# Kernel tuning notes

Hardware: AMD Instinct MI355X
Metric: run time of the kernel (lower is better)

## Reference

```python
import jax, jax.numpy as jnp
import numpy as np

B, Q, K = 4, 256, 1024          # batch, query_len, key_len
DQ, DK, DV, H = 512, 512, 512, 256  # query/key/value dims, num_hiddens


def setup_inputs() -> dict:
    key = jax.random.key(0)
    ks = jax.random.split(key, 7)
    return {
        "queries": jax.random.normal(ks[0], (B, Q, DQ), jnp.float32),
        "keys": jax.random.normal(ks[1], (B, K, DK), jnp.float32),
        "values": jax.random.normal(ks[2], (B, K, DV), jnp.float32),
        "valid_lens": jax.random.randint(ks[3], (B,), 1, K + 1),
        "Wq": jax.random.normal(ks[4], (H, DQ), jnp.float32) / np.sqrt(DQ).astype(np.float32),
        "Wk": jax.random.normal(ks[5], (H, DK), jnp.float32) / np.sqrt(DK).astype(np.float32),
        "wv": jax.random.normal(ks[6], (H,), jnp.float32) / np.sqrt(H).astype(np.float32),
    }


def reference(queries, keys, values, valid_lens, Wq, Wk, wv):
    # Linear projections (bias=False), torch Linear weight layout (out, in)
    q = jnp.einsum("bqd,hd->bqh", queries, Wq)          # (B, Q, H)
    k = jnp.einsum("bkd,hd->bkh", keys, Wk)             # (B, K, H)
    # Broadcast add -> tanh -> scalar score per (q, k) pair
    feats = jnp.tanh(q[:, :, None, :] + k[:, None, :, :])  # (B, Q, K, H)
    scores = jnp.einsum("bqkh,h->bqk", feats, wv)           # (B, Q, K)
    # masked_softmax with 1D valid_lens: mask applies along key axis per batch
    kv_len = scores.shape[-1]
    mask = jnp.arange(kv_len)[None, None, :] < valid_lens[:, None, None]  # (B,1,K)
    scores = jnp.where(mask, scores, jnp.float32(-1e6))
    attn = jax.nn.softmax(scores, axis=-1)               # (B, Q, K)
    # dropout is identity in eval mode
    return jnp.einsum("bqk,bkv->bqv", attn, values)      # (B, Q, DV)
```

## Files before the change

### kernel.cpp

```cpp
#include <hip/hip_runtime.h>
#include <stdint.h>


#define NB 4
#define NQ 256
#define NK 1024
#define ND 512
#define NH 256
#define QROWS 4
#define PJR 16
#define PJH 64

#define C2L2E 2.8853900817779268f
#define L2E   1.4426950408889634f

typedef float v2f __attribute__((ext_vector_type(2)));

__device__ void ff_vldec(const int* p, int* v) {
  bool ok = true;
  for (int i = 0; i < 4; ++i) { int x = p[i]; if (x < 1 || x > NK) ok = false; }
  if (ok) { for (int i = 0; i < 4; ++i) v[i] = p[i]; return; }
  ok = true;
  for (int i = 0; i < 4; ++i) {
    if (p[2 * i + 1] != 0) ok = false;
    int x = p[2 * i]; if (x < 1 || x > NK) ok = false;
  }
  if (ok) { for (int i = 0; i < 4; ++i) v[i] = p[2 * i]; return; }
  ok = true;
  for (int i = 0; i < 4; ++i) {
    union { int i; float f; } u; u.i = p[i];
    if (!(u.f >= 1.0f && u.f <= 1024.0f && u.f == floorf(u.f))) ok = false;
  }
  if (ok) {
    for (int i = 0; i < 4; ++i) { union { int i; float f; } u; u.i = p[i]; v[i] = (int)u.f; }
    return;
  }
  ok = true;
  for (int i = 0; i < 4; ++i) {
    union { long long l; double d; } u;
    u.l = ((long long)p[2 * i + 1] << 32) | (unsigned int)p[2 * i];
    if (!(u.d >= 1.0 && u.d <= 1024.0 && u.d == floor(u.d))) ok = false;
  }
  if (ok) {
    for (int i = 0; i < 4; ++i) {
      union { long long l; double d; } u;
      u.l = ((long long)p[2 * i + 1] << 32) | (unsigned int)p[2 * i];
      v[i] = (int)u.d;
    }
    return;
  }
  const uint16_t* hh = (const uint16_t*)p;
  const short*    s  = (const short*)p;
  ok = true;
  for (int i = 0; i < 4; ++i) { int x = s[i]; if (x < 1 || x > NK) ok = false; }
  if (ok) { for (int i = 0; i < 4; ++i) v[i] = s[i]; return; }
  ok = true;
  for (int i = 0; i < 4; ++i) {
    union { uint16_t u; _Float16 h; } u; u.u = hh[i];
    float f = (float)u.h;
    if (!(f >= 1.0f && f <= 1024.0f && f == floorf(f))) ok = false;
  }
  if (ok) {
    for (int i = 0; i < 4; ++i) {
      union { uint16_t u; _Float16 h; } u; u.u = hh[i];
      v[i] = (int)(float)u.h;
    }
    return;
  }
  ok = true;
  for (int i = 0; i < 4; ++i) {
    union { uint32_t u; float f; } u; u.u = ((uint32_t)hh[i]) << 16;
    if (!(u.f >= 1.0f && u.f <= 1028.0f)) ok = false;
  }
  if (ok) {
    for (int i = 0; i < 4; ++i) {
      union { uint32_t u; float f; } u; u.u = ((uint32_t)hh[i]) << 16;
      int x = (int)(u.f + 0.5f); if (x > NK) x = NK; v[i] = x;
    }
    return;
  }
  for (int i = 0; i < 4; ++i) v[i] = NK;
}

__global__ __launch_bounds__(256) void ff_wt(
    const float* __restrict__ Wq, const float* __restrict__ Wk,
    float* __restrict__ WTq, float* __restrict__ WTk)
{
  const int idx = blockIdx.x * 256 + threadIdx.x;
  const int d4 = idx & 127, h = idx >> 7;
  const float* src = blockIdx.y ? Wk : Wq;
  float*       dst = blockIdx.y ? WTk : WTq;
  float4 w = *(const float4*)(src + (size_t)h * ND + d4 * 4);
  w.x *= C2L2E; w.y *= C2L2E; w.z *= C2L2E; w.w *= C2L2E;
  *(float4*)(dst + ((size_t)d4 * NH + h) * 4) = w;
}

__global__ __launch_bounds__(256) void ff_proj(
    const float* __restrict__ q_in, const float* __restrict__ k_in,
    const float* __restrict__ WTq, const float* __restrict__ WTk,
    float* __restrict__ qp, float* __restrict__ kp)
{
  __shared__ float xs[PJR * ND];
  const int t  = threadIdx.x;
  const int rg = blockIdx.x >> 2;
  const int h0 = (blockIdx.x & 3) * PJH;
  const int gr0 = rg * PJR;
  const bool isq = gr0 < NB * NQ;
  const float* xin = isq ? (q_in + (size_t)gr0 * ND)
                         : (k_in + (size_t)(gr0 - NB * NQ) * ND);
  const float4* wt4 = (const float4*)(isq ? WTq : WTk);

  #pragma unroll
  for (int i = 0; i < 8; ++i)
    ((float4*)xs)[t + 256 * i] = ((const float4*)xin)[t + 256 * i];
  __syncthreads();

  const int L  = t & 63;
  const int rw = t >> 6;
  float a0 = 0.f, a1 = 0.f, a2 = 0.f, a3 = 0.f;
  const float4* xr = (const float4*)xs + (size_t)(4 * rw) * 128;

  #pragma unroll 4
  for (int d4 = 0; d4 < ND / 4; ++d4) {
    float4 w  = wt4[(size_t)d4 * NH + h0 + L];
    float4 x0 = xr[d4];
    float4 x1 = xr[128 + d4];
    float4 x2 = xr[256 + d4];
    float4 x3 = xr[384 + d4];
    a0 += w.x*x0.x + w.y*x0.y + w.z*x0.z + w.w*x0.w;
    a1 += w.x*x1.x + w.y*x1.y + w.z*x1.z + w.w*x1.w;
    a2 += w.x*x2.x + w.y*x2.y + w.z*x2.z + w.w*x2.w;
    a3 += w.x*x3.x + w.y*x3.y + w.z*x3.z + w.w*x3.w;
  }
  a0 = __builtin_amdgcn_exp2f(a0);
  a1 = __builtin_amdgcn_exp2f(a1);
  a2 = __builtin_amdgcn_exp2f(a2);
  a3 = __builtin_amdgcn_exp2f(a3);

  if (isq) {
    const int h = h0 + L;
    float* o = qp + (size_t)(gr0 + 4 * rw) * NH + h;
    o[0] = a0; o[NH] = a1; o[2 * NH] = a2; o[3 * NH] = a3;
  } else {
    __syncthreads();
    float* trs = xs;
    *(float4*)&trs[L * 16 + 4 * rw] = make_float4(a0, a1, a2, a3);
    __syncthreads();
    const int kl = t & 15, jl = t >> 4;
    const int g0 = gr0 - NB * NQ;
    const int bb = g0 >> 10, kg0 = g0 & (NK - 1);
    const int j0 = (blockIdx.x & 3) * 16;
    float4 o4 = make_float4(trs[(4*jl+0)*16 + kl], trs[(4*jl+1)*16 + kl],
                            trs[(4*jl+2)*16 + kl], trs[(4*jl+3)*16 + kl]);
    ((float4*)kp)[((size_t)bb * 64 + j0 + jl) * 1024 + kg0 + kl] = o4;
  }
}

__global__ __launch_bounds__(1024, 8) void ff_attn_s(
    const float* __restrict__ qp, const float* __restrict__ kp,
    const int* __restrict__ vlraw, const float* __restrict__ wvp,
    float* __restrict__ Eg, float* __restrict__ Sg)
{
  __shared__ float  qs[QROWS * NH];
  __shared__ float4 wspp[NH / 2];
  __shared__ float  el[512 * 4];
  __shared__ float  psum[32];

  const int t  = threadIdx.x;
  const int kh = blockIdx.x;
  const int q4 = blockIdx.y;
  const int b  = blockIdx.z;

  qs[t] = qp[((size_t)b * NQ + q4 * QROWS) * NH + t];
  if (t < NH / 2) {
    float w0 = wvp[2 * t], w1 = wvp[2 * t + 1];
    wspp[t] = make_float4(-2.0f * w0, -2.0f * w1, -2.0f * (w0 + w1), 0.0f);
  }
  __syncthreads();

  int vls[4];
  ff_vldec(vlraw, vls);
  const int vl = vls[b];

  const int l  = t & 63, w = t >> 6;
  const int hs = l >> 4, kl = l & 15;
  const int kw = w & 7,  rh = w >> 3;
  const int kk = kw * 16 + kl;
  const int k0 = kh * 512 + kk * 4;

  v2f acc0 = {0.f,0.f}, acc1 = {0.f,0.f}, acc2 = {0.f,0.f}, acc3 = {0.f,0.f};
  {
    const float4* kvp = (const float4*)kp + (size_t)b * 64 * 1024 + k0;
    const float* q0p = qs + (2 * rh) * NH;
    const float* q1p = qs + (2 * rh + 1) * NH;

    for (int jj = 0; jj < 16; ++jj) {
      const int j = hs * 16 + jj;
      const float4* kj = kvp + ((size_t)j << 10);
      float4 K0 = kj[0], K1 = kj[1], K2 = kj[2], K3 = kj[3];
      float4 A0 = *(const float4*)(q0p + 4 * j);
      float4 A1 = *(const float4*)(q1p + 4 * j);
      float4 wa = wspp[2 * j];
      float4 wb = wspp[2 * j + 1];
      v2f one; one.x = 1.0f; one.y = 1.0f;

#define FF_PAIRK(K4, ACC)                                                  \
      {                                                                    \
        v2f a, b2, D, N, w0v, w1v, rD;                                     \
        a.x  = A0.x * K4.x; a.y  = A1.x * K4.x;                            \
        b2.x = A0.y * K4.y; b2.y = A1.y * K4.y;                            \
        D = (one + a) * (one + b2);                                        \
        N.x = wa.z; N.y = wa.z;                                            \
        w0v.x = wa.x; w0v.y = wa.x;                                        \
        w1v.x = wa.y; w1v.y = wa.y;                                        \
        N += w0v * b2; N += w1v * a;                                       \
        rD.x = __builtin_amdgcn_rcpf(D.x);                                 \
        rD.y = __builtin_amdgcn_rcpf(D.y);                                 \
        ACC += N * rD;                                                     \
        a.x  = A0.z * K4.z; a.y  = A1.z * K4.z;                            \
        b2.x = A0.w * K4.w; b2.y = A1.w * K4.w;                            \
        D = (one + a) * (one + b2);                                        \
        N.x = wb.z; N.y = wb.z;                                            \
        w0v.x = wb.x; w0v.y = wb.x;                                        \
        w1v.x = wb.y; w1v.y = wb.y;                                        \
        N += w0v * b2; N += w1v * a;                                       \
        rD.x = __builtin_amdgcn_rcpf(D.x);                                 \
        rD.y = __builtin_amdgcn_rcpf(D.y);                                 \
        ACC += N * rD;                                                     \
      }
      FF_PAIRK(K0, acc0)
      FF_PAIRK(K1, acc1)
      FF_PAIRK(K2, acc2)
      FF_PAIRK(K3, acc3)
#undef FF_PAIRK
    }
  }

#define FF_RED(v)                                                          \
  v.x += __shfl_xor(v.x, 16); v.x += __shfl_xor(v.x, 32);                  \
  v.y += __shfl_xor(v.y, 16); v.y += __shfl_xor(v.y, 32);
  FF_RED(acc0) FF_RED(acc1) FF_RED(acc2) FF_RED(acc3)
#undef FF_RED

  float ex0, ey0, ex1, ey1, ex2, ey2, ex3, ey3;
  {
    const bool m0 = (k0 + 0) < vl, m1 = (k0 + 1) < vl;
    const bool m2 = (k0 + 2) < vl, m3 = (k0 + 3) < vl;
    ex0 = m0 ? __builtin_amdgcn_exp2f(acc0.x * L2E) : 0.f;
    ey0 = m0 ? __builtin_amdgcn_exp2f(acc0.y * L2E) : 0.f;
    ex1 = m1 ? __builtin_amdgcn_exp2f(acc1.x * L2E) : 0.f;
    ey1 = m1 ? __builtin_amdgcn_exp2f(acc1.y * L2E) : 0.f;
    ex2 = m2 ? __builtin_amdgcn_exp2f(acc2.x * L2E) : 0.f;
    ey2 = m2 ? __builtin_amdgcn_exp2f(acc2.y * L2E) : 0.f;
    ex3 = m3 ? __builtin_amdgcn_exp2f(acc3.x * L2E) : 0.f;
    ey3 = m3 ? __builtin_amdgcn_exp2f(acc3.y * L2E) : 0.f;
  }

  if (hs == 0) {
    const int klc = kk * 4;
    el[(klc + 0) * 4 + 2 * rh] = ex0; el[(klc + 0) * 4 + 2 * rh + 1] = ey0;
    el[(klc + 1) * 4 + 2 * rh] = ex1; el[(klc + 1) * 4 + 2 * rh + 1] = ey1;
    el[(klc + 2) * 4 + 2 * rh] = ex2; el[(klc + 2) * 4 + 2 * rh + 1] = ey2;
    el[(klc + 3) * 4 + 2 * rh] = ex3; el[(klc + 3) * 4 + 2 * rh + 1] = ey3;
  }
  {
    float sl = (hs == 0) ? ((ex0 + ex1) + (ex2 + ex3)) : 0.f;
    float sh = (hs == 0) ? ((ey0 + ey1) + (ey2 + ey3)) : 0.f;
    for (int o = 32; o; o >>= 1) { sl += __shfl_xor(sl, o); sh += __shfl_xor(sh, o); }
    if (l == 0) { psum[w * 2] = sl; psum[w * 2 + 1] = sh; }
  }
  __syncthreads();

  if (t < 512)
    ((float4*)Eg)[((size_t)b * 64 + q4) * NK + kh * 512 + t]
        = *(const float4*)&el[t * 4];

  if (t < 4) {
    const int c = t & 1, base = (t >> 1) * 8;
    float S = 0.f;
    #pragma unroll
    for (int kw2 = 0; kw2 < 8; ++kw2) S += psum[(base + kw2) * 2 + c];
    Sg[(((size_t)b * 64 + q4) * 4 + t) * 2 + kh] = S;
  }
}

__global__ __launch_bounds__(256) void ff_pv(
    const float* __restrict__ vals, const float* __restrict__ Eg,
    const float* __restrict__ Sg, const int* __restrict__ vlraw,
    float* __restrict__ out)
{
  __shared__ float part[8 * 4 * 64];
  const int t  = threadIdx.x;
  const int ct = blockIdx.x;
  const int q4 = blockIdx.y;
  const int b  = blockIdx.z;

  int vls[4];
  ff_vldec(vlraw, vls);
  const int vl = vls[b];

  const int cl = t & 31, kq = t >> 5;
  const int c  = ct * 64 + cl * 2;
  const int k0 = kq * 128;
  int klen = vl - k0; klen = klen < 0 ? 0 : (klen > 128 ? 128 : klen);

  const float*  vb = vals + (size_t)b * NK * ND + (size_t)k0 * ND + c;
  const float4* ep = (const float4*)Eg + ((size_t)b * 64 + q4) * NK + k0;

  v2f a0 = {0.f,0.f}, a1 = {0.f,0.f}, a2 = {0.f,0.f}, a3 = {0.f,0.f};
  #pragma unroll 4
  for (int k = 0; k < klen; ++k) {
    float4 E = ep[k];
    v2f v = *(const v2f*)(vb + (size_t)k * ND);
    v2f e;
    e.x = E.x; e.y = E.x; a0 += e * v;
    e.x = E.y; e.y = E.y; a1 += e * v;
    e.x = E.z; e.y = E.z; a2 += e * v;
    e.x = E.w; e.y = E.w; a3 += e * v;
  }
  {
    float* pp = &part[(size_t)(kq * 4) * 64 + cl * 2];
    *(v2f*)(pp      ) = a0;
    *(v2f*)(pp + 64 ) = a1;
    *(v2f*)(pp + 128) = a2;
    *(v2f*)(pp + 192) = a3;
  }
  __syncthreads();
  {
    const int r = t >> 6, cc = t & 63;
    float s = 0.f;
    #pragma unroll
    for (int q = 0; q < 8; ++q) s += part[(size_t)(q * 4 + r) * 64 + cc];
    const size_t sb = ((size_t)b * 64 + q4) * 4 + r;
    const float S = Sg[sb * 2] + Sg[sb * 2 + 1];
    out[((size_t)b * NQ + q4 * QROWS + r) * ND + ct * 64 + cc] = s / S;
  }
}

__global__ __launch_bounds__(1024) void ff_attn(
    const float* __restrict__ qp, const float* __restrict__ kp,
    const float* __restrict__ vals, const int* __restrict__ vlraw,
    const float* __restrict__ wvp, float* __restrict__ out)
{
  __shared__ float qs[QROWS * NH];
  __shared__ float ws[NH];
  __shared__ float st[NK * QROWS];
  __shared__ float pm[16], psm[16];
  __shared__ float part[4 * QROWS * ND];

  const int t  = threadIdx.x;
  const int q0 = blockIdx.x * QROWS;
  const int b  = blockIdx.y;

  {
    const float* qsrc = qp + ((size_t)b * NQ + q0) * NH;
    qs[t] = qsrc[t];
    if (t < NH) ws[t] = -2.0f * wvp[t];
  }
  __syncthreads();

  int vls[4];
  ff_vldec(vlraw, vls);
  const int vl = vls[b];

  float sc[4] = {0.f, 0.f, 0.f, 0.f};
  {
    const float4* kvp = (const float4*)kp + ((size_t)b * 64) * 1024 + t;
    for (int j = 0; j < 64; ++j) {
      float4 K4 = kvp[(size_t)j << 10];
      const float* wj = &ws[4 * j];
      #pragma unroll
      for (int r = 0; r < 4; ++r) {
        const float* qr = &qs[r * NH + 4 * j];
        sc[r] += wj[0] * __builtin_amdgcn_rcpf(1.0f + qr[0] * K4.x);
        sc[r] += wj[1] * __builtin_amdgcn_rcpf(1.0f + qr[1] * K4.y);
        sc[r] += wj[2] * __builtin_amdgcn_rcpf(1.0f + qr[2] * K4.z);
        sc[r] += wj[3] * __builtin_amdgcn_rcpf(1.0f + qr[3] * K4.w);
      }
    }
  }
  {
    const bool okm = (t < vl);
    *(float4*)&st[t * 4] = make_float4(okm ? sc[0] : -1e6f, okm ? sc[1] : -1e6f,
                                       okm ? sc[2] : -1e6f, okm ? sc[3] : -1e6f);
  }
  __syncthreads();

  {
    const int wid = t >> 6, lane = t & 63;
    const int row = wid >> 2, seg = wid & 3;
    const int kb = seg * 256 + lane;
    float v0 = st[(kb      ) * 4 + row];
    float v1 = st[(kb +  64) * 4 + row];
    float v2 = st[(kb + 128) * 4 + row];
    float v3 = st[(kb + 192) * 4 + row];
    float m = fmaxf(fmaxf(v0, v1), fmaxf(v2, v3));
    for (int o = 32; o; o >>= 1) m = fmaxf(m, __shfl_xor(m, o));
    if (lane == 0) pm[wid] = m;
    __syncthreads();
    m = fmaxf(fmaxf(pm[row*4+0], pm[row*4+1]), fmaxf(pm[row*4+2], pm[row*4+3]));
    float e0 = __builtin_amdgcn_exp2f((v0 - m) * L2E);
    float e1 = __builtin_amdgcn_exp2f((v1 - m) * L2E);
    float e2 = __builtin_amdgcn_exp2f((v2 - m) * L2E);
    float e3 = __builtin_amdgcn_exp2f((v3 - m) * L2E);
    float sm = e0 + e1 + e2 + e3;
    for (int o = 32; o; o >>= 1) sm += __shfl_xor(sm, o);
    if (lane == 0) psm[wid] = sm;
    __syncthreads();
    const float S = psm[row*4+0] + psm[row*4+1] + psm[row*4+2] + psm[row*4+3];
    const float rr = 1.0f / S;
    st[(kb      ) * 4 + row] = e0 * rr;
    st[(kb +  64) * 4 + row] = e1 * rr;
    st[(kb + 128) * 4 + row] = e2 * rr;
    st[(kb + 192) * 4 + row] = e3 * rr;
  }
  __syncthreads();

  {
    const int kq = t >> 8, c2 = (t & 255) * 2;
    const float* vb = vals + (size_t)b * NK * ND + c2;
    v2f o0 = {0.f,0.f}, o1 = {0.f,0.f}, o2 = {0.f,0.f}, o3 = {0.f,0.f};
    const int k0 = kq * 256;
    #pragma unroll 8
    for (int k = k0; k < k0 + 256; ++k) {
      v2f vv = *(const v2f*)(vb + (size_t)k * ND);
      float4 a = *(const float4*)&st[k * 4];
      v2f ax; ax.x = a.x; ax.y = a.x;
      v2f ay; ay.x = a.y; ay.y = a.y;
      v2f az; az.x = a.z; az.y = a.z;
      v2f aw; aw.x = a.w; aw.y = a.w;
      o0 += ax * vv; o1 += ay * vv; o2 += az * vv; o3 += aw * vv;
    }
    float* pp = &part[(size_t)kq * QROWS * ND + c2];
    *(v2f*)(pp         ) = o0;
    *(v2f*)(pp +     ND) = o1;
    *(v2f*)(pp + 2 * ND) = o2;
    *(v2f*)(pp + 3 * ND) = o3;
  }
  __syncthreads();
  {
    const int r = t >> 8, c2 = (t & 255) * 2;
    const float* pp = &part[(size_t)r * ND + c2];
    v2f s = {0.f, 0.f};
    #pragma unroll
    for (int kq = 0; kq < 4; ++kq) s += *(const v2f*)(pp + (size_t)kq * QROWS * ND);
    *(v2f*)(out + ((size_t)b * NQ + q0 + r) * ND + c2) = s;
  }
}

extern "C" void kernel_launch(void* const* d_in, const int* in_sizes, int n_in,
                              void* d_out, int out_size, void* d_ws, size_t ws_size,
                              hipStream_t stream) {
  const float* queries = (const float*)d_in[0];
  const float* keys    = (const float*)d_in[1];
  const float* values  = (const float*)d_in[2];
  const int*   vlens   = (const int*)d_in[3];
  const float* Wq      = (const float*)d_in[4];
  const float* Wk      = (const float*)d_in[5];
  const float* wv      = (const float*)d_in[6];
  float* out = (float*)d_out;

  float* qp  = (float*)d_ws;
  float* kp  = qp  + (size_t)NB * NQ * NH;
  float* wtq = kp  + (size_t)NB * NH * NK;
  float* wtk = wtq + (size_t)(ND / 4) * NH * 4;
  float* Eg  = wtk + (size_t)(ND / 4) * NH * 4;
  float* Sg  = Eg  + (size_t)NB * 64 * NK * 4;
  const size_t need = ((size_t)(Sg - (float*)d_ws) + NB * 64 * 4 * 2) * sizeof(float);

  ff_wt  <<<dim3(128, 2), 256, 0, stream>>>(Wq, Wk, wtq, wtk);
  ff_proj<<<dim3((NB * (NQ + NK) / PJR) * (NH / PJH)), 256, 0, stream>>>(
      queries, keys, wtq, wtk, qp, kp);
  if (ws_size >= need) {
    ff_attn_s<<<dim3(2, NQ / QROWS, NB), 1024, 0, stream>>>(
        qp, kp, vlens, wv, Eg, Sg);
    ff_pv<<<dim3(8, NQ / QROWS, NB), 256, 0, stream>>>(
        values, Eg, Sg, vlens, out);
  } else {
    ff_attn<<<dim3(NQ / QROWS, NB), 1024, 0, stream>>>(
        qp, kp, values, vlens, wv, out);
  }
}
```

Before: 174.7 us.

## Widen per-block tiles in projection and PV kernels, pad LDS to avoid conflicts

The projection kernel now computes 128 hidden columns per block instead of 64, so each staged input row tile is reused across twice as many outputs and half as many blocks reload it. The PV kernel handles two query groups per block, reusing each loaded value vector for eight query rows and halving value-matrix traffic. The LDS transpose buffers in the projection and score kernels are padded (stride 17 and 5) to reduce bank conflicts. In exchange, register pressure rises and there are fewer blocks to fill the GPU.

Result: slower. 183.8 us (+5.2%).

```diff
diff --git a/kernel.cpp b/kernel.cpp
--- a/kernel.cpp
+++ b/kernel.cpp
@@ -9,7 +9,6 @@
 #define NH 256
 #define QROWS 4
 #define PJR 16
-#define PJH 64
 
 #define C2L2E 2.8853900817779268f
 #define L2E   1.4426950408889634f
@@ -102,8 +101,8 @@
 {
   __shared__ float xs[PJR * ND];
   const int t  = threadIdx.x;
-  const int rg = blockIdx.x >> 2;
-  const int h0 = (blockIdx.x & 3) * PJH;
+  const int rg = blockIdx.x >> 1;
+  const int hh = blockIdx.x & 1;
   const int gr0 = rg * PJR;
   const bool isq = gr0 < NB * NQ;
   const float* xin = isq ? (q_in + (size_t)gr0 * ND)
@@ -117,42 +116,58 @@
 
   const int L  = t & 63;
   const int rw = t >> 6;
-  float a0 = 0.f, a1 = 0.f, a2 = 0.f, a3 = 0.f;
+  float ac0[4], ac1[4];
+  #pragma unroll
+  for (int r = 0; r < 4; ++r) { ac0[r] = 0.f; ac1[r] = 0.f; }
   const float4* xr = (const float4*)xs + (size_t)(4 * rw) * 128;
+  const int hbase = hh * 128 + L;
 
   #pragma unroll 4
   for (int d4 = 0; d4 < ND / 4; ++d4) {
-    float4 w  = wt4[(size_t)d4 * NH + h0 + L];
+    float4 w0 = wt4[(size_t)d4 * NH + hbase];
+    float4 w1 = wt4[(size_t)d4 * NH + hbase + 64];
     float4 x0 = xr[d4];
     float4 x1 = xr[128 + d4];
     float4 x2 = xr[256 + d4];
     float4 x3 = xr[384 + d4];
-    a0 += w.x*x0.x + w.y*x0.y + w.z*x0.z + w.w*x0.w;
-    a1 += w.x*x1.x + w.y*x1.y + w.z*x1.z + w.w*x1.w;
-    a2 += w.x*x2.x + w.y*x2.y + w.z*x2.z + w.w*x2.w;
-    a3 += w.x*x3.x + w.y*x3.y + w.z*x3.z + w.w*x3.w;
-  }
-  a0 = __builtin_amdgcn_exp2f(a0);
-  a1 = __builtin_amdgcn_exp2f(a1);
-  a2 = __builtin_amdgcn_exp2f(a2);
-  a3 = __builtin_amdgcn_exp2f(a3);
+    ac0[0] += w0.x*x0.x + w0.y*x0.y + w0.z*x0.z + w0.w*x0.w;
+    ac0[1] += w0.x*x1.x + w0.y*x1.y + w0.z*x1.z + w0.w*x1.w;
+    ac0[2] += w0.x*x2.x + w0.y*x2.y + w0.z*x2.z + w0.w*x2.w;
+    ac0[3] += w0.x*x3.x + w0.y*x3.y + w0.z*x3.z + w0.w*x3.w;
+    ac1[0] += w1.x*x0.x + w1.y*x0.y + w1.z*x0.z + w1.w*x0.w;
+    ac1[1] += w1.x*x1.x + w1.y*x1.y + w1.z*x1.z + w1.w*x1.w;
+    ac1[2] += w1.x*x2.x + w1.y*x2.y + w1.z*x2.z + w1.w*x2.w;
+    ac1[3] += w1.x*x3.x + w1.y*x3.y + w1.z*x3.z + w1.w*x3.w;
+  }
+  #pragma unroll
+  for (int r = 0; r < 4; ++r) {
+    ac0[r] = __builtin_amdgcn_exp2f(ac0[r]);
+    ac1[r] = __builtin_amdgcn_exp2f(ac1[r]);
+  }
 
   if (isq) {
-    const int h = h0 + L;
-    float* o = qp + (size_t)(gr0 + 4 * rw) * NH + h;
-    o[0] = a0; o[NH] = a1; o[2 * NH] = a2; o[3 * NH] = a3;
+    float* o = qp + (size_t)(gr0 + 4 * rw) * NH + hh * 128 + L;
+    #pragma unroll
+    for (int r = 0; r < 4; ++r) {
+      o[(size_t)r * NH]      = ac0[r];
+      o[(size_t)r * NH + 64] = ac1[r];
+    }
   } else {
     __syncthreads();
     float* trs = xs;
-    *(float4*)&trs[L * 16 + 4 * rw] = make_float4(a0, a1, a2, a3);
+    *(float4*)&trs[(L     ) * 17 + 4 * rw] = make_float4(ac0[0], ac0[1], ac0[2], ac0[3]);
+    *(float4*)&trs[(L + 64) * 17 + 4 * rw] = make_float4(ac1[0], ac1[1], ac1[2], ac1[3]);
     __syncthreads();
-    const int kl = t & 15, jl = t >> 4;
+    const int kl = t & 15, jl2 = t >> 4;
     const int g0 = gr0 - NB * NQ;
     const int bb = g0 >> 10, kg0 = g0 & (NK - 1);
-    const int j0 = (blockIdx.x & 3) * 16;
-    float4 o4 = make_float4(trs[(4*jl+0)*16 + kl], trs[(4*jl+1)*16 + kl],
-                            trs[(4*jl+2)*16 + kl], trs[(4*jl+3)*16 + kl]);
-    ((float4*)kp)[((size_t)bb * 64 + j0 + jl) * 1024 + kg0 + kl] = o4;
+    #pragma unroll
+    for (int it = 0; it < 2; ++it) {
+      const int jl = jl2 + 16 * it;
+      float4 o4 = make_float4(trs[(4*jl+0)*17 + kl], trs[(4*jl+1)*17 + kl],
+                              trs[(4*jl+2)*17 + kl], trs[(4*jl+3)*17 + kl]);
+      ((float4*)kp)[((size_t)bb * 64 + hh * 32 + jl) * 1024 + kg0 + kl] = o4;
+    }
   }
 }
 
@@ -163,7 +178,7 @@
 {
   __shared__ float  qs[QROWS * NH];
   __shared__ float4 wspp[NH / 2];
-  __shared__ float  el[512 * 4];
+  __shared__ float  el[512 * 5];
   __shared__ float  psum[32];
 
   const int t  = threadIdx.x;
@@ -258,10 +273,10 @@
 
   if (hs == 0) {
     const int klc = kk * 4;
-    el[(klc + 0) * 4 + 2 * rh] = ex0; el[(klc + 0) * 4 + 2 * rh + 1] = ey0;
-    el[(klc + 1) * 4 + 2 * rh] = ex1; el[(klc + 1) * 4 + 2 * rh + 1] = ey1;
-    el[(klc + 2) * 4 + 2 * rh] = ex2; el[(klc + 2) * 4 + 2 * rh + 1] = ey2;
-    el[(klc + 3) * 4 + 2 * rh] = ex3; el[(klc + 3) * 4 + 2 * rh + 1] = ey3;
+    el[(klc + 0) * 5 + 2 * rh] = ex0; el[(klc + 0) * 5 + 2 * rh + 1] = ey0;
+    el[(klc + 1) * 5 + 2 * rh] = ex1; el[(klc + 1) * 5 + 2 * rh + 1] = ey1;
+    el[(klc + 2) * 5 + 2 * rh] = ex2; el[(klc + 2) * 5 + 2 * rh + 1] = ey2;
+    el[(klc + 3) * 5 + 2 * rh] = ex3; el[(klc + 3) * 5 + 2 * rh + 1] = ey3;
   }
   {
     float sl = (hs == 0) ? ((ex0 + ex1) + (ex2 + ex3)) : 0.f;
@@ -271,9 +286,11 @@
   }
   __syncthreads();
 
-  if (t < 512)
+  if (t < 512) {
+    const float* e = &el[t * 5];
     ((float4*)Eg)[((size_t)b * 64 + q4) * NK + kh * 512 + t]
-        = *(const float4*)&el[t * 4];
+        = make_float4(e[0], e[1], e[2], e[3]);
+  }
 
   if (t < 4) {
     const int c = t & 1, base = (t >> 1) * 8;
@@ -289,10 +306,10 @@
     const float* __restrict__ Sg, const int* __restrict__ vlraw,
     float* __restrict__ out)
 {
-  __shared__ float part[8 * 4 * 64];
+  __shared__ float part[8 * 8 * 64];
   const int t  = threadIdx.x;
   const int ct = blockIdx.x;
-  const int q4 = blockIdx.y;
+  const int qg = blockIdx.y;
   const int b  = blockIdx.z;
 
   int vls[4];
@@ -304,36 +321,52 @@
   const int k0 = kq * 128;
   int klen = vl - k0; klen = klen < 0 ? 0 : (klen > 128 ? 128 : klen);
 
-  const float*  vb = vals + (size_t)b * NK * ND + (size_t)k0 * ND + c;
-  const float4* ep = (const float4*)Eg + ((size_t)b * 64 + q4) * NK + k0;
+  const float*  vb  = vals + (size_t)b * NK * ND + (size_t)k0 * ND + c;
+  const float4* epa = (const float4*)Eg + ((size_t)b * 64 + qg * 2    ) * NK + k0;
+  const float4* epb = (const float4*)Eg + ((size_t)b * 64 + qg * 2 + 1) * NK + k0;
 
   v2f a0 = {0.f,0.f}, a1 = {0.f,0.f}, a2 = {0.f,0.f}, a3 = {0.f,0.f};
+  v2f a4 = {0.f,0.f}, a5 = {0.f,0.f}, a6 = {0.f,0.f}, a7 = {0.f,0.f};
   #pragma unroll 4
   for (int k = 0; k < klen; ++k) {
-    float4 E = ep[k];
+    float4 Ea = epa[k];
+    float4 Eb = epb[k];
     v2f v = *(const v2f*)(vb + (size_t)k * ND);
     v2f e;
-    e.x = E.x; e.y = E.x; a0 += e * v;
-    e.x = E.y; e.y = E.y; a1 += e * v;
-    e.x = E.z; e.y = E.z; a2 += e * v;
-    e.x = E.w; e.y = E.w; a3 += e * v;
-  }
-  {
-    float* pp = &part[(size_t)(kq * 4) * 64 + cl * 2];
+    e.x = Ea.x; e.y = Ea.x; a0 += e * v;
+    e.x = Ea.y; e.y = Ea.y; a1 += e * v;
+    e.x = Ea.z; e.y = Ea.z; a2 += e * v;
+    e.x = Ea.w; e.y = Ea.w; a3 += e * v;
+    e.x = Eb.x; e.y = Eb.x; a4 += e * v;
+    e.x = Eb.y; e.y = Eb.y; a5 += e * v;
+    e.x = Eb.z; e.y = Eb.z; a6 += e * v;
+    e.x = Eb.w; e.y = Eb.w; a7 += e * v;
+  }
+  {
+    float* pp = &part[(size_t)(kq * 8) * 64 + cl * 2];
     *(v2f*)(pp      ) = a0;
     *(v2f*)(pp + 64 ) = a1;
     *(v2f*)(pp + 128) = a2;
     *(v2f*)(pp + 192) = a3;
-  }
-  __syncthreads();
-  {
-    const int r = t >> 6, cc = t & 63;
-    float s = 0.f;
+    *(v2f*)(pp + 256) = a4;
+    *(v2f*)(pp + 320) = a5;
+    *(v2f*)(pp + 384) = a6;
+    *(v2f*)(pp + 448) = a7;
+  }
+  __syncthreads();
+  {
+    const int cc = t & 63;
     #pragma unroll
-    for (int q = 0; q < 8; ++q) s += part[(size_t)(q * 4 + r) * 64 + cc];
-    const size_t sb = ((size_t)b * 64 + q4) * 4 + r;
-    const float S = Sg[sb * 2] + Sg[sb * 2 + 1];
-    out[((size_t)b * NQ + q4 * QROWS + r) * ND + ct * 64 + cc] = s / S;
+    for (int rr = 0; rr < 2; ++rr) {
+      const int row = (t >> 6) * 2 + rr;
+      float s = 0.f;
+      #pragma unroll
+      for (int q = 0; q < 8; ++q) s += part[(size_t)(q * 8 + row) * 64 + cc];
+      const int q4 = qg * 2 + (row >> 2), r = row & 3;
+      const size_t sb = ((size_t)b * 64 + q4) * 4 + r;
+      const float S = Sg[sb * 2] + Sg[sb * 2 + 1];
+      out[((size_t)b * NQ + q4 * QROWS + r) * ND + ct * 64 + cc] = s / S;
+    }
   }
 }
 
@@ -469,12 +502,12 @@
   const size_t need = ((size_t)(Sg - (float*)d_ws) + NB * 64 * 4 * 2) * sizeof(float);
 
   ff_wt  <<<dim3(128, 2), 256, 0, stream>>>(Wq, Wk, wtq, wtk);
-  ff_proj<<<dim3((NB * (NQ + NK) / PJR) * (NH / PJH)), 256, 0, stream>>>(
+  ff_proj<<<dim3((NB * (NQ + NK) / PJR) * 2), 256, 0, stream>>>(
       queries, keys, wtq, wtk, qp, kp);
   if (ws_size >= need) {
     ff_attn_s<<<dim3(2, NQ / QROWS, NB), 1024, 0, stream>>>(
         qp, kp, vlens, wv, Eg, Sg);
-    ff_pv<<<dim3(8, NQ / QROWS, NB), 256, 0, stream>>>(
+    ff_pv<<<dim3(8, NQ / (QROWS * 2), NB), 256, 0, stream>>>(
         values, Eg, Sg, vlens, out);
   } else {
     ff_attn<<<dim3(NQ / QROWS, NB), 1024, 0, stream>>>(
```

## Process eight query rows per PV block and pad exp staging buffer

Applied to the files above, without the earlier changes.

The PV kernel now handles two 4-row query groups per block, so each loaded value vector is reused across eight rows, halving value-tensor reads and the block count. Separately, the exp staging buffer in the score kernel is padded to stride 5 to reduce LDS bank conflicts on the scattered writes, at the cost of scalar reads when building the float4 output. The wider PV tile doubles accumulators and shared memory per block and halves grid parallelism.

After: 181.7 us. 4.0% more time.

```diff
diff --git a/kernel.cpp b/kernel.cpp
--- a/kernel.cpp
+++ b/kernel.cpp
@@ -163,7 +163,7 @@
 {
   __shared__ float  qs[QROWS * NH];
   __shared__ float4 wspp[NH / 2];
-  __shared__ float  el[512 * 4];
+  __shared__ float  el[512 * 5];
   __shared__ float  psum[32];
 
   const int t  = threadIdx.x;
@@ -258,10 +258,10 @@
 
   if (hs == 0) {
     const int klc = kk * 4;
-    el[(klc + 0) * 4 + 2 * rh] = ex0; el[(klc + 0) * 4 + 2 * rh + 1] = ey0;
-    el[(klc + 1) * 4 + 2 * rh] = ex1; el[(klc + 1) * 4 + 2 * rh + 1] = ey1;
-    el[(klc + 2) * 4 + 2 * rh] = ex2; el[(klc + 2) * 4 + 2 * rh + 1] = ey2;
-    el[(klc + 3) * 4 + 2 * rh] = ex3; el[(klc + 3) * 4 + 2 * rh + 1] = ey3;
+    el[(klc + 0) * 5 + 2 * rh] = ex0; el[(klc + 0) * 5 + 2 * rh + 1] = ey0;
+    el[(klc + 1) * 5 + 2 * rh] = ex1; el[(klc + 1) * 5 + 2 * rh + 1] = ey1;
+    el[(klc + 2) * 5 + 2 * rh] = ex2; el[(klc + 2) * 5 + 2 * rh + 1] = ey2;
+    el[(klc + 3) * 5 + 2 * rh] = ex3; el[(klc + 3) * 5 + 2 * rh + 1] = ey3;
   }
   {
     float sl = (hs == 0) ? ((ex0 + ex1) + (ex2 + ex3)) : 0.f;
@@ -271,9 +271,11 @@
   }
   __syncthreads();
 
-  if (t < 512)
+  if (t < 512) {
+    const float* e = &el[t * 5];
     ((float4*)Eg)[((size_t)b * 64 + q4) * NK + kh * 512 + t]
-        = *(const float4*)&el[t * 4];
+        = make_float4(e[0], e[1], e[2], e[3]);
+  }
 
   if (t < 4) {
     const int c = t & 1, base = (t >> 1) * 8;
@@ -289,10 +291,10 @@
     const float* __restrict__ Sg, const int* __restrict__ vlraw,
     float* __restrict__ out)
 {
-  __shared__ float part[8 * 4 * 64];
+  __shared__ float part[8 * 8 * 64];
   const int t  = threadIdx.x;
   const int ct = blockIdx.x;
-  const int q4 = blockIdx.y;
+  const int qg = blockIdx.y;
   const int b  = blockIdx.z;
 
   int vls[4];
@@ -304,36 +306,52 @@
   const int k0 = kq * 128;
   int klen = vl - k0; klen = klen < 0 ? 0 : (klen > 128 ? 128 : klen);
 
-  const float*  vb = vals + (size_t)b * NK * ND + (size_t)k0 * ND + c;
-  const float4* ep = (const float4*)Eg + ((size_t)b * 64 + q4) * NK + k0;
+  const float*  vb  = vals + (size_t)b * NK * ND + (size_t)k0 * ND + c;
+  const float4* epa = (const float4*)Eg + ((size_t)b * 64 + qg * 2    ) * NK + k0;
+  const float4* epb = (const float4*)Eg + ((size_t)b * 64 + qg * 2 + 1) * NK + k0;
 
   v2f a0 = {0.f,0.f}, a1 = {0.f,0.f}, a2 = {0.f,0.f}, a3 = {0.f,0.f};
+  v2f a4 = {0.f,0.f}, a5 = {0.f,0.f}, a6 = {0.f,0.f}, a7 = {0.f,0.f};
   #pragma unroll 4
   for (int k = 0; k < klen; ++k) {
-    float4 E = ep[k];
+    float4 Ea = epa[k];
+    float4 Eb = epb[k];
     v2f v = *(const v2f*)(vb + (size_t)k * ND);
     v2f e;
-    e.x = E.x; e.y = E.x; a0 += e * v;
-    e.x = E.y; e.y = E.y; a1 += e * v;
-    e.x = E.z; e.y = E.z; a2 += e * v;
-    e.x = E.w; e.y = E.w; a3 += e * v;
-  }
-  {
-    float* pp = &part[(size_t)(kq * 4) * 64 + cl * 2];
+    e.x = Ea.x; e.y = Ea.x; a0 += e * v;
+    e.x = Ea.y; e.y = Ea.y; a1 += e * v;
+    e.x = Ea.z; e.y = Ea.z; a2 += e * v;
+    e.x = Ea.w; e.y = Ea.w; a3 += e * v;
+    e.x = Eb.x; e.y = Eb.x; a4 += e * v;
+    e.x = Eb.y; e.y = Eb.y; a5 += e * v;
+    e.x = Eb.z; e.y = Eb.z; a6 += e * v;
+    e.x = Eb.w; e.y = Eb.w; a7 += e * v;
+  }
+  {
+    float* pp = &part[(size_t)(kq * 8) * 64 + cl * 2];
     *(v2f*)(pp      ) = a0;
     *(v2f*)(pp + 64 ) = a1;
     *(v2f*)(pp + 128) = a2;
     *(v2f*)(pp + 192) = a3;
-  }
-  __syncthreads();
-  {
-    const int r = t >> 6, cc = t & 63;
-    float s = 0.f;
+    *(v2f*)(pp + 256) = a4;
+    *(v2f*)(pp + 320) = a5;
+    *(v2f*)(pp + 384) = a6;
+    *(v2f*)(pp + 448) = a7;
+  }
+  __syncthreads();
+  {
+    const int cc = t & 63;
     #pragma unroll
-    for (int q = 0; q < 8; ++q) s += part[(size_t)(q * 4 + r) * 64 + cc];
-    const size_t sb = ((size_t)b * 64 + q4) * 4 + r;
-    const float S = Sg[sb * 2] + Sg[sb * 2 + 1];
-    out[((size_t)b * NQ + q4 * QROWS + r) * ND + ct * 64 + cc] = s / S;
+    for (int rr = 0; rr < 2; ++rr) {
+      const int row = (t >> 6) * 2 + rr;
+      float s = 0.f;
+      #pragma unroll
+      for (int q = 0; q < 8; ++q) s += part[(size_t)(q * 8 + row) * 64 + cc];
+      const int q4 = qg * 2 + (row >> 2), r = row & 3;
+      const size_t sb = ((size_t)b * 64 + q4) * 4 + r;
+      const float S = Sg[sb * 2] + Sg[sb * 2 + 1];
+      out[((size_t)b * NQ + q4 * QROWS + r) * ND + ct * 64 + cc] = s / S;
+    }
   }
 }
 
@@ -474,7 +492,7 @@
   if (ws_size >= need) {
     ff_attn_s<<<dim3(2, NQ / QROWS, NB), 1024, 0, stream>>>(
         qp, kp, vlens, wv, Eg, Sg);
-    ff_pv<<<dim3(8, NQ / QROWS, NB), 256, 0, stream>>>(
+    ff_pv<<<dim3(8, NQ / (QROWS * 2), NB), 256, 0, stream>>>(
         values, Eg, Sg, vlens, out);
   } else {
     ff_attn<<<dim3(NQ / QROWS, NB), 1024, 0, stream>>>(
```
